# Performance work log

Hardware: AMD Instinct MI355X
Metric: run time of the kernel (lower is better)

Reference implementation:

```python
import jax, jax.numpy as jnp
import numpy as np

N_HEAD, D_MODEL, D_K, D_V = 16, 1024, 64, 64
BATCH, SEQ = 4, 2048


def setup_inputs() -> dict:
    key = jax.random.key(0)
    ks = jax.random.split(key, 9)
    s = 1.0 / np.sqrt(D_MODEL)
    so = 1.0 / np.sqrt(N_HEAD * D_V)
    inp = {
        "input": jax.random.normal(ks[0], (BATCH, SEQ, D_MODEL), jnp.float32),
        # causal mask: True => masked (set to -inf), matching masked_fill semantics
        "attn_mask": jnp.triu(jnp.ones((SEQ, SEQ), bool), k=1),
        "Wq": jax.random.uniform(ks[1], (D_MODEL, N_HEAD * D_K), jnp.float32, -s, s),
        "bq": jax.random.uniform(ks[2], (N_HEAD * D_K,), jnp.float32, -s, s),
        "Wk": jax.random.uniform(ks[3], (D_MODEL, N_HEAD * D_K), jnp.float32, -s, s),
        "bk": jax.random.uniform(ks[4], (N_HEAD * D_K,), jnp.float32, -s, s),
        "Wv": jax.random.uniform(ks[5], (D_MODEL, N_HEAD * D_V), jnp.float32, -s, s),
        "bv": jax.random.uniform(ks[6], (N_HEAD * D_V,), jnp.float32, -s, s),
        "Wo": jax.random.uniform(ks[7], (N_HEAD * D_V, D_MODEL), jnp.float32, -so, so),
        "bo": jax.random.uniform(ks[8], (D_MODEL,), jnp.float32, -so, so),
    }
    return inp


def reference(input, attn_mask, Wq, bq, Wk, bk, Wv, bv, Wo, bo):
    B, S, _ = input.shape
    scale = 1.0 / np.sqrt(D_K)
    q = (input @ Wq + bq).reshape(B, S, N_HEAD, D_K)  # bshd
    k = (input @ Wk + bk).reshape(B, S, N_HEAD, D_K)
    v = (input @ Wv + bv).reshape(B, S, N_HEAD, D_V)
    # scores [B, H, S, S]
    score = jnp.einsum("bqhd,bkhd->bhqk", q, k) * scale
    score = jnp.where(attn_mask[None, None], -jnp.inf, score)
    prob = jax.nn.softmax(score, axis=-1)
    attn = jnp.einsum("bhqk,bkhd->bqhd", prob, v).reshape(B, S, N_HEAD * D_V)
    return attn @ Wo + bo
```

## Files before the change

### kernel.cpp

```cpp
#include <hip/hip_runtime.h>
#include <math.h>


typedef __attribute__((ext_vector_type(8))) short short8;
typedef __attribute__((ext_vector_type(4))) short s16x4;
typedef __attribute__((ext_vector_type(4))) float f32x4;
typedef __attribute__((ext_vector_type(4))) unsigned short u16x4;

constexpr int B  = 4;
constexpr int S  = 2048;
constexpr int H  = 16;
constexpr int DM = 1024;
constexpr int M  = B * S;

__device__ __forceinline__ unsigned short f2bf(float f) {
    union { float f; unsigned u; } v; v.f = f;
    unsigned r = v.u + 0x7FFFu + ((v.u >> 16) & 1u);
    return (unsigned short)(r >> 16);
}

__device__ __forceinline__ void gload16(const void* g, void* l) {
    __builtin_amdgcn_global_load_lds(
        (const __attribute__((address_space(1))) void*)g,
        (__attribute__((address_space(3))) void*)l, 16, 0, 0);
}

__device__ __forceinline__ f32x4 mfma_16x16x16(s16x4 a, s16x4 b, f32x4 c) {
#if __has_builtin(__builtin_amdgcn_mfma_f32_16x16x16bf16_1k)
    return __builtin_amdgcn_mfma_f32_16x16x16bf16_1k(a, b, c, 0, 0, 0);
#else
    asm("v_mfma_f32_16x16x16_bf16 %0, %1, %2, %0" : "+v"(c) : "v"(a), "v"(b));
    return c;
#endif
}

__global__ __launch_bounds__(256) void cast_x_kernel(
    const float* __restrict__ in, unsigned short* __restrict__ out)
{
    const size_t i = (size_t)blockIdx.x * 256 + threadIdx.x;
    const float4* p = (const float4*)in;
    float4 a = p[2 * i], b = p[2 * i + 1];
    short8 o;
    o[0] = (short)f2bf(a.x); o[1] = (short)f2bf(a.y);
    o[2] = (short)f2bf(a.z); o[3] = (short)f2bf(a.w);
    o[4] = (short)f2bf(b.x); o[5] = (short)f2bf(b.y);
    o[6] = (short)f2bf(b.z); o[7] = (short)f2bf(b.w);
    *(short8*)(out + 8 * i) = o;
}

__global__ __launch_bounds__(256) void transpose_cast_w(
    const float* __restrict__ W, unsigned short* __restrict__ Wt)
{
    __shared__ float tile[32][33];
    const int t = threadIdx.x;
    const int r0 = blockIdx.y * 32, c0 = blockIdx.x * 32;
    {
        const int r = t >> 3, c4 = (t & 7) * 4;
        float4 a = *(const float4*)&W[(size_t)(r0 + r) * 1024 + c0 + c4];
        tile[r][c4 + 0] = a.x; tile[r][c4 + 1] = a.y;
        tile[r][c4 + 2] = a.z; tile[r][c4 + 3] = a.w;
    }
    __syncthreads();
    {
        const int n = t >> 3, k4 = (t & 7) * 4;
        u16x4 o;
        o[0] = f2bf(tile[k4 + 0][n]); o[1] = f2bf(tile[k4 + 1][n]);
        o[2] = f2bf(tile[k4 + 2][n]); o[3] = f2bf(tile[k4 + 3][n]);
        *(u16x4*)&Wt[(size_t)(c0 + n) * 1024 + r0 + k4] = o;
    }
}

template <int MODE>
__global__ __launch_bounds__(256) void gemm_bf16(
    const unsigned short* __restrict__ X, const unsigned short* __restrict__ Wt,
    const float* __restrict__ bias, void* __restrict__ dst, float scale)
{
    __shared__ __align__(16) unsigned short As[128 * 32];
    __shared__ __align__(16) unsigned short Bs[128 * 32];

    const int t = threadIdx.x;
    const int lane = t & 63, w = t >> 6;
    const int wr = w >> 1, wc = w & 1;
    const int l15 = lane & 15, lhi = lane >> 4;
    const int row0 = blockIdx.y * 128, col0 = blockIdx.x * 128;

    const f32x4 z = {0.f, 0.f, 0.f, 0.f};
    f32x4 acc[4][4];
    #pragma unroll
    for (int i = 0; i < 4; ++i)
        #pragma unroll
        for (int j = 0; j < 4; ++j) acc[i][j] = z;

    const int fchunk = ((lhi ^ ((l15 >> 1) & 3)) << 4);

    for (int k0 = 0; k0 < 1024; k0 += 32) {
        __syncthreads();
        #pragma unroll
        for (int i = 0; i < 2; ++i) {
            int seg = t + i * 256;
            int row = seg >> 2;
            int ch  = (seg & 3) ^ ((row >> 1) & 3);
            gload16(X  + (size_t)(row0 + row) * 1024 + k0 + ch * 8, (char*)As + seg * 16);
            gload16(Wt + (size_t)(col0 + row) * 1024 + k0 + ch * 8, (char*)Bs + seg * 16);
        }
        __syncthreads();

        short8 a[4], b[4];
        #pragma unroll
        for (int mi = 0; mi < 4; ++mi)
            a[mi] = *(const short8*)((const char*)As + (wr * 64 + mi * 16 + l15) * 64 + fchunk);
        #pragma unroll
        for (int ni = 0; ni < 4; ++ni)
            b[ni] = *(const short8*)((const char*)Bs + (wc * 64 + ni * 16 + l15) * 64 + fchunk);
        #pragma unroll
        for (int mi = 0; mi < 4; ++mi)
            #pragma unroll
            for (int ni = 0; ni < 4; ++ni)
                acc[mi][ni] = __builtin_amdgcn_mfma_f32_16x16x32_bf16(
                    a[mi], b[ni], acc[mi][ni], 0, 0, 0);
    }

    #pragma unroll
    for (int mi = 0; mi < 4; ++mi)
        #pragma unroll
        for (int ni = 0; ni < 4; ++ni) {
            const int cc = col0 + wc * 64 + ni * 16 + l15;
            const float bv = bias[cc];
            if constexpr (MODE == 2) {
                const int rr0 = row0 + wr * 64 + mi * 16 + lhi * 4;
                const int b0 = rr0 >> 11, s0_ = rr0 & 2047;
                u16x4 pv;
                pv[0] = f2bf(acc[mi][ni][0] + bv);
                pv[1] = f2bf(acc[mi][ni][1] + bv);
                pv[2] = f2bf(acc[mi][ni][2] + bv);
                pv[3] = f2bf(acc[mi][ni][3] + bv);
                *(u16x4*)&((unsigned short*)dst)[
                    (((size_t)(b0 * 16 + (cc >> 6)) * 64 + (cc & 63)) << 11) + s0_] = pv;
            } else {
                #pragma unroll
                for (int r = 0; r < 4; ++r) {
                    const int rr = row0 + wr * 64 + mi * 16 + lhi * 4 + r;
                    const float val = acc[mi][ni][r] + bv;
                    if constexpr (MODE == 0) {
                        ((unsigned short*)dst)[((((size_t)(rr >> 11) * 16 + (cc >> 6)) * 2048
                                                + (rr & 2047)) << 6) + (cc & 63)]
                            = f2bf(val * scale);
                    } else {
                        ((float*)dst)[(size_t)rr * 1024 + cc] = val;
                    }
                }
            }
        }
}

__global__ __launch_bounds__(256) void attn_mfma(
    const unsigned short* __restrict__ Q, const unsigned short* __restrict__ K,
    const unsigned short* __restrict__ Vt, unsigned short* __restrict__ Out)
{
    __shared__ __align__(16) unsigned short Ks[2][64 * 64];
    __shared__ __align__(16) unsigned short Vs[2][64 * 64];

    const int t = threadIdx.x, lane = t & 63, w = t >> 6;
    const int l15 = lane & 15, lhi = lane >> 4;
    const int id = blockIdx.x;
    const int bx = id >> 6, bh = id & 63;
    const int q0 = bx * 128;
    const size_t base = (size_t)bh * S * 64;

    short8 bq[2][2];
    #pragma unroll
    for (int mi = 0; mi < 2; ++mi)
        #pragma unroll
        for (int ks = 0; ks < 2; ++ks)
            bq[mi][ks] = *(const short8*)(Q + base
                + (size_t)(q0 + w * 32 + mi * 16 + l15) * 64 + ks * 32 + lhi * 8);

    const f32x4 z = {0.f, 0.f, 0.f, 0.f};
    f32x4 o[2][4];
    float mrow[2] = {-INFINITY, -INFINITY}, lrow[2] = {0.f, 0.f};
    #pragma unroll
    for (int mi = 0; mi < 2; ++mi)
        #pragma unroll
        for (int d = 0; d < 4; ++d) o[mi][d] = z;

    auto STAGE = [&](int buf, int kt) {
        const int k0 = kt * 64;
        #pragma unroll
        for (int i = 0; i < 2; ++i) {
            int seg = t + i * 256;
            int row = seg >> 3;
            int ch  = (seg & 7) ^ (row & 7);
            gload16(K + base + (size_t)(k0 + row) * 64 + ch * 8,
                    (char*)Ks[buf] + seg * 16);
            gload16(Vt + ((size_t)bh * 64 + row) * S + k0 + ch * 8,
                    (char*)Vs[buf] + seg * 16);
        }
    };

    const int ntiles = 2 * bx + 2;
    STAGE(0, 0);
    __syncthreads();

    for (int kt = 0; kt < ntiles; ++kt) {
        const int cur = kt & 1;
        const int k0 = kt * 64;
        if (kt + 1 < ntiles) STAGE(cur ^ 1, kt + 1);

        f32x4 sc[2][4];
        #pragma unroll
        for (int mi = 0; mi < 2; ++mi)
            #pragma unroll
            for (int ni = 0; ni < 4; ++ni) sc[mi][ni] = z;
        #pragma unroll
        for (int ks = 0; ks < 2; ++ks)
            #pragma unroll
            for (int ni = 0; ni < 4; ++ni) {
                short8 ak = *(const short8*)((const char*)Ks[cur]
                    + (ni * 16 + l15) * 128 + (((ks * 4 + lhi) ^ (l15 & 7)) << 4));
                #pragma unroll
                for (int mi = 0; mi < 2; ++mi)
                    sc[mi][ni] = __builtin_amdgcn_mfma_f32_16x16x32_bf16(
                        ak, bq[mi][ks], sc[mi][ni], 0, 0, 0);
            }

        if (k0 >= q0) {
            #pragma unroll
            for (int mi = 0; mi < 2; ++mi) {
                const int qg = q0 + w * 32 + mi * 16 + l15;
                #pragma unroll
                for (int ni = 0; ni < 4; ++ni)
                    #pragma unroll
                    for (int r = 0; r < 4; ++r)
                        if (k0 + ni * 16 + lhi * 4 + r > qg)
                            sc[mi][ni][r] = -INFINITY;
            }
        }

        s16x4 pf[2][4];
        #pragma unroll
        for (int mi = 0; mi < 2; ++mi) {
            float tm = -INFINITY;
            #pragma unroll
            for (int ni = 0; ni < 4; ++ni) {
                float a0 = fmaxf(sc[mi][ni][0], sc[mi][ni][1]);
                float a1 = fmaxf(sc[mi][ni][2], sc[mi][ni][3]);
                tm = fmaxf(tm, fmaxf(a0, a1));
            }
            tm = fmaxf(tm, __shfl_xor(tm, 16));
            tm = fmaxf(tm, __shfl_xor(tm, 32));
            const float mnew = fmaxf(mrow[mi], tm);
            const float alpha = exp2f(mrow[mi] - mnew);
            mrow[mi] = mnew;
            float ps = 0.f;
            #pragma unroll
            for (int ni = 0; ni < 4; ++ni) {
                #pragma unroll
                for (int r = 0; r < 4; ++r) {
                    float pp = exp2f(sc[mi][ni][r] - mnew);
                    sc[mi][ni][r] = pp;
                    ps += pp;
                }
                s16x4 pk;
                pk[0] = (short)f2bf(sc[mi][ni][0]);
                pk[1] = (short)f2bf(sc[mi][ni][1]);
                pk[2] = (short)f2bf(sc[mi][ni][2]);
                pk[3] = (short)f2bf(sc[mi][ni][3]);
                pf[mi][ni] = pk;
            }
            ps += __shfl_xor(ps, 16);
            ps += __shfl_xor(ps, 32);
            lrow[mi] = lrow[mi] * alpha + ps;
            #pragma unroll
            for (int d = 0; d < 4; ++d) {
                o[mi][d][0] *= alpha; o[mi][d][1] *= alpha;
                o[mi][d][2] *= alpha; o[mi][d][3] *= alpha;
            }
        }

        #pragma unroll
        for (int ni = 0; ni < 4; ++ni) {
            #pragma unroll
            for (int db = 0; db < 4; ++db) {
                const int row = db * 16 + l15;
                const int slot = ((ni * 2 + (lhi >> 1)) ^ (l15 & 7));
                s16x4 av = *(const s16x4*)((const char*)Vs[cur]
                    + row * 128 + slot * 16 + (lhi & 1) * 8);
                #pragma unroll
                for (int mi = 0; mi < 2; ++mi)
                    o[mi][db] = mfma_16x16x16(av, pf[mi][ni], o[mi][db]);
            }
        }

        __syncthreads();
    }

    const int b_ = bh >> 4, h_ = bh & 15;
    #pragma unroll
    for (int mi = 0; mi < 2; ++mi) {
        const float inv = 1.0f / lrow[mi];
        const int s_ = q0 + w * 32 + mi * 16 + l15;
        #pragma unroll
        for (int db = 0; db < 4; ++db) {
            u16x4 ov;
            ov[0] = f2bf(o[mi][db][0] * inv);
            ov[1] = f2bf(o[mi][db][1] * inv);
            ov[2] = f2bf(o[mi][db][2] * inv);
            ov[3] = f2bf(o[mi][db][3] * inv);
            *(u16x4*)&Out[(size_t)(b_ * S + s_) * 1024 + h_ * 64 + db * 16 + lhi * 4] = ov;
        }
    }
}

extern "C" void kernel_launch(void* const* d_in, const int* in_sizes, int n_in,
                              void* d_out, int out_size, void* d_ws, size_t ws_size,
                              hipStream_t stream)
{
    const float* x  = (const float*)d_in[0];
    const float* Wq = (const float*)d_in[2];
    const float* bq = (const float*)d_in[3];
    const float* Wk = (const float*)d_in[4];
    const float* bk = (const float*)d_in[5];
    const float* Wv = (const float*)d_in[6];
    const float* bv = (const float*)d_in[7];
    const float* Wo = (const float*)d_in[8];
    const float* bo = (const float*)d_in[9];
    float* out = (float*)d_out;

    unsigned short* p = (unsigned short*)d_ws;
    unsigned short* xb  = p; p += (size_t)M * DM;
    unsigned short* wqt = p; p += (size_t)DM * DM;
    unsigned short* wkt = p; p += (size_t)DM * DM;
    unsigned short* wvt = p; p += (size_t)DM * DM;
    unsigned short* wot = p; p += (size_t)DM * DM;
    unsigned short* qb  = p; p += (size_t)M * DM;
    unsigned short* kb  = p; p += (size_t)M * DM;
    unsigned short* vtb = p; p += (size_t)M * DM;
    unsigned short* attnb = p;

    cast_x_kernel<<<M * DM / 8 / 256, 256, 0, stream>>>(x, xb);
    transpose_cast_w<<<dim3(32, 32), 256, 0, stream>>>(Wq, wqt);
    transpose_cast_w<<<dim3(32, 32), 256, 0, stream>>>(Wk, wkt);
    transpose_cast_w<<<dim3(32, 32), 256, 0, stream>>>(Wv, wvt);
    transpose_cast_w<<<dim3(32, 32), 256, 0, stream>>>(Wo, wot);

    const float qscale = 0.125f * 1.44269504088896340736f;
    gemm_bf16<0><<<dim3(8, 64), 256, 0, stream>>>(xb, wqt, bq, qb, qscale);
    gemm_bf16<0><<<dim3(8, 64), 256, 0, stream>>>(xb, wkt, bk, kb, 1.0f);
    gemm_bf16<2><<<dim3(8, 64), 256, 0, stream>>>(xb, wvt, bv, vtb, 1.0f);

    attn_mfma<<<dim3(1024), 256, 0, stream>>>(qb, kb, vtb, attnb);

    gemm_bf16<1><<<dim3(8, 64), 256, 0, stream>>>(attnb, wot, bo, out, 1.0f);
}
```

Measured before the change: 351.0 us.

## Fuse QKV projections, double-buffer GEMM, lazy softmax rescale, packed bf16 conversion

Merges the Q, K and V projection GEMMs into one launch over a 3072-wide output. This relies on the three transposed weight buffers sitting next to each other in the workspace, and picks the bias and destination per column range. The four weight transpose launches become one 3D-grid launch. The GEMM main loop now double-buffers its LDS tiles so the next k-slice loads while the current one computes. In attention, the online-softmax rescale of O and l is skipped unless the running max grows by more than 8 in log2 space. Softmax and output bf16 packing use v_cvt_pk_bf16_f32, and the V^T store is swizzled so LDS reads hit fewer bank conflicts. These changes add LDS use per GEMM block and slightly change numerics through lazy rescaling and hardware rounding.

Measured after the change: 314.5 us. 10.4% less time.

```diff
diff --git a/kernel.cpp b/kernel.cpp
--- a/kernel.cpp
+++ b/kernel.cpp
@@ -6,6 +6,7 @@
 typedef __attribute__((ext_vector_type(4))) short s16x4;
 typedef __attribute__((ext_vector_type(4))) float f32x4;
 typedef __attribute__((ext_vector_type(4))) unsigned short u16x4;
+typedef __attribute__((ext_vector_type(2))) unsigned int u32x2;
 
 constexpr int B  = 4;
 constexpr int S  = 2048;
@@ -17,6 +18,14 @@
     union { float f; unsigned u; } v; v.f = f;
     unsigned r = v.u + 0x7FFFu + ((v.u >> 16) & 1u);
     return (unsigned short)(r >> 16);
+}
+
+__device__ __forceinline__ s16x4 pack_bf16x4(float a, float b, float c, float d) {
+    unsigned r0, r1;
+    asm("v_cvt_pk_bf16_f32 %0, %1, %2" : "=v"(r0) : "v"(a), "v"(b));
+    asm("v_cvt_pk_bf16_f32 %0, %1, %2" : "=v"(r1) : "v"(c), "v"(d));
+    u32x2 t; t[0] = r0; t[1] = r1;
+    return __builtin_bit_cast(s16x4, t);
 }
 
 __device__ __forceinline__ void gload16(const void* g, void* l) {
@@ -49,8 +58,15 @@
 }
 
 __global__ __launch_bounds__(256) void transpose_cast_w(
-    const float* __restrict__ W, unsigned short* __restrict__ Wt)
-{
+    const float* __restrict__ W0, const float* __restrict__ W1,
+    const float* __restrict__ W2, const float* __restrict__ W3,
+    unsigned short* __restrict__ T0, unsigned short* __restrict__ T1,
+    unsigned short* __restrict__ T2, unsigned short* __restrict__ T3)
+{
+    const int z = blockIdx.z;
+    const float* W = (z == 0) ? W0 : (z == 1) ? W1 : (z == 2) ? W2 : W3;
+    unsigned short* Wt = (z == 0) ? T0 : (z == 1) ? T1 : (z == 2) ? T2 : T3;
+
     __shared__ float tile[32][33];
     const int t = threadIdx.x;
     const int r0 = blockIdx.y * 32, c0 = blockIdx.x * 32;
@@ -70,13 +86,16 @@
     }
 }
 
-template <int MODE>
+template <int FUSED>
 __global__ __launch_bounds__(256) void gemm_bf16(
     const unsigned short* __restrict__ X, const unsigned short* __restrict__ Wt,
-    const float* __restrict__ bias, void* __restrict__ dst, float scale)
-{
-    __shared__ __align__(16) unsigned short As[128 * 32];
-    __shared__ __align__(16) unsigned short Bs[128 * 32];
+    const float* __restrict__ bias_q, const float* __restrict__ bias_k,
+    const float* __restrict__ bias_v,
+    void* __restrict__ dq, void* __restrict__ dk, void* __restrict__ dv,
+    float qscale)
+{
+    __shared__ __align__(16) unsigned short As[2][128 * 32];
+    __shared__ __align__(16) unsigned short Bs[2][128 * 32];
 
     const int t = threadIdx.x;
     const int lane = t & 63, w = t >> 6;
@@ -93,25 +112,34 @@
 
     const int fchunk = ((lhi ^ ((l15 >> 1) & 3)) << 4);
 
-    for (int k0 = 0; k0 < 1024; k0 += 32) {
-        __syncthreads();
+    auto STAGE = [&](int buf, int k0) {
         #pragma unroll
         for (int i = 0; i < 2; ++i) {
             int seg = t + i * 256;
             int row = seg >> 2;
             int ch  = (seg & 3) ^ ((row >> 1) & 3);
-            gload16(X  + (size_t)(row0 + row) * 1024 + k0 + ch * 8, (char*)As + seg * 16);
-            gload16(Wt + (size_t)(col0 + row) * 1024 + k0 + ch * 8, (char*)Bs + seg * 16);
-        }
+            gload16(X  + (size_t)(row0 + row) * 1024 + k0 + ch * 8,
+                    (char*)As[buf] + seg * 16);
+            gload16(Wt + (size_t)(col0 + row) * 1024 + k0 + ch * 8,
+                    (char*)Bs[buf] + seg * 16);
+        }
+    };
+
+    STAGE(0, 0);
+    for (int k0 = 0; k0 < 1024; k0 += 32) {
+        const int cur = (k0 >> 5) & 1;
         __syncthreads();
+        if (k0 + 32 < 1024) STAGE(cur ^ 1, k0 + 32);
 
         short8 a[4], b[4];
         #pragma unroll
         for (int mi = 0; mi < 4; ++mi)
-            a[mi] = *(const short8*)((const char*)As + (wr * 64 + mi * 16 + l15) * 64 + fchunk);
+            a[mi] = *(const short8*)((const char*)As[cur]
+                + (wr * 64 + mi * 16 + l15) * 64 + fchunk);
         #pragma unroll
         for (int ni = 0; ni < 4; ++ni)
-            b[ni] = *(const short8*)((const char*)Bs + (wc * 64 + ni * 16 + l15) * 64 + fchunk);
+            b[ni] = *(const short8*)((const char*)Bs[cur]
+                + (wc * 64 + ni * 16 + l15) * 64 + fchunk);
         #pragma unroll
         for (int mi = 0; mi < 4; ++mi)
             #pragma unroll
@@ -125,29 +153,34 @@
         #pragma unroll
         for (int ni = 0; ni < 4; ++ni) {
             const int cc = col0 + wc * 64 + ni * 16 + l15;
-            const float bv = bias[cc];
-            if constexpr (MODE == 2) {
+            if constexpr (FUSED == 1) {
+                const int sel = cc >> 10;
+                const int hh = (cc >> 6) & 15, dd = cc & 63;
+                const float bv = (sel == 0 ? bias_q : sel == 1 ? bias_k : bias_v)
+                                 [cc & 1023];
                 const int rr0 = row0 + wr * 64 + mi * 16 + lhi * 4;
-                const int b0 = rr0 >> 11, s0_ = rr0 & 2047;
-                u16x4 pv;
-                pv[0] = f2bf(acc[mi][ni][0] + bv);
-                pv[1] = f2bf(acc[mi][ni][1] + bv);
-                pv[2] = f2bf(acc[mi][ni][2] + bv);
-                pv[3] = f2bf(acc[mi][ni][3] + bv);
-                *(u16x4*)&((unsigned short*)dst)[
-                    (((size_t)(b0 * 16 + (cc >> 6)) * 64 + (cc & 63)) << 11) + s0_] = pv;
+                const int b0i = rr0 >> 11, s0_ = rr0 & 2047;
+                if (sel == 2) {
+                    const int sstore = s0_ ^ (((cc >> 3) & 1) << 2);
+                    s16x4 pv = pack_bf16x4(
+                        acc[mi][ni][0] + bv, acc[mi][ni][1] + bv,
+                        acc[mi][ni][2] + bv, acc[mi][ni][3] + bv);
+                    *(s16x4*)&((unsigned short*)dv)[
+                        (((size_t)(b0i * 16 + hh) * 64 + dd) << 11) + sstore] = pv;
+                } else {
+                    unsigned short* dst = (unsigned short*)(sel == 0 ? dq : dk);
+                    const float sc_ = (sel == 0) ? qscale : 1.0f;
+                    #pragma unroll
+                    for (int r = 0; r < 4; ++r)
+                        dst[(((size_t)(b0i * 16 + hh) * 2048 + s0_ + r) << 6) + dd]
+                            = f2bf((acc[mi][ni][r] + bv) * sc_);
+                }
             } else {
+                const float bv = bias_q[cc];
                 #pragma unroll
                 for (int r = 0; r < 4; ++r) {
                     const int rr = row0 + wr * 64 + mi * 16 + lhi * 4 + r;
-                    const float val = acc[mi][ni][r] + bv;
-                    if constexpr (MODE == 0) {
-                        ((unsigned short*)dst)[((((size_t)(rr >> 11) * 16 + (cc >> 6)) * 2048
-                                                + (rr & 2047)) << 6) + (cc & 63)]
-                            = f2bf(val * scale);
-                    } else {
-                        ((float*)dst)[(size_t)rr * 1024 + cc] = val;
-                    }
+                    ((float*)dq)[(size_t)rr * 1024 + cc] = acc[mi][ni][r] + bv;
                 }
             }
         }
@@ -248,33 +281,30 @@
             }
             tm = fmaxf(tm, __shfl_xor(tm, 16));
             tm = fmaxf(tm, __shfl_xor(tm, 32));
-            const float mnew = fmaxf(mrow[mi], tm);
-            const float alpha = exp2f(mrow[mi] - mnew);
-            mrow[mi] = mnew;
+            if (!__all(tm <= mrow[mi] + 8.f)) {
+                const float mnew = fmaxf(mrow[mi], tm);
+                const float alpha = exp2f(mrow[mi] - mnew);
+                mrow[mi] = mnew;
+                lrow[mi] *= alpha;
+                #pragma unroll
+                for (int d = 0; d < 4; ++d) {
+                    o[mi][d][0] *= alpha; o[mi][d][1] *= alpha;
+                    o[mi][d][2] *= alpha; o[mi][d][3] *= alpha;
+                }
+            }
             float ps = 0.f;
             #pragma unroll
             for (int ni = 0; ni < 4; ++ni) {
-                #pragma unroll
-                for (int r = 0; r < 4; ++r) {
-                    float pp = exp2f(sc[mi][ni][r] - mnew);
-                    sc[mi][ni][r] = pp;
-                    ps += pp;
-                }
-                s16x4 pk;
-                pk[0] = (short)f2bf(sc[mi][ni][0]);
-                pk[1] = (short)f2bf(sc[mi][ni][1]);
-                pk[2] = (short)f2bf(sc[mi][ni][2]);
-                pk[3] = (short)f2bf(sc[mi][ni][3]);
-                pf[mi][ni] = pk;
+                float p0 = exp2f(sc[mi][ni][0] - mrow[mi]);
+                float p1 = exp2f(sc[mi][ni][1] - mrow[mi]);
+                float p2 = exp2f(sc[mi][ni][2] - mrow[mi]);
+                float p3 = exp2f(sc[mi][ni][3] - mrow[mi]);
+                ps += (p0 + p1) + (p2 + p3);
+                pf[mi][ni] = pack_bf16x4(p0, p1, p2, p3);
             }
             ps += __shfl_xor(ps, 16);
             ps += __shfl_xor(ps, 32);
-            lrow[mi] = lrow[mi] * alpha + ps;
-            #pragma unroll
-            for (int d = 0; d < 4; ++d) {
-                o[mi][d][0] *= alpha; o[mi][d][1] *= alpha;
-                o[mi][d][2] *= alpha; o[mi][d][3] *= alpha;
-            }
+            lrow[mi] += ps;
         }
 
         #pragma unroll
@@ -283,8 +313,9 @@
             for (int db = 0; db < 4; ++db) {
                 const int row = db * 16 + l15;
                 const int slot = ((ni * 2 + (lhi >> 1)) ^ (l15 & 7));
+                const int half = (lhi & 1) ^ ((l15 >> 3) & 1);
                 s16x4 av = *(const s16x4*)((const char*)Vs[cur]
-                    + row * 128 + slot * 16 + (lhi & 1) * 8);
+                    + row * 128 + slot * 16 + half * 8);
                 #pragma unroll
                 for (int mi = 0; mi < 2; ++mi)
                     o[mi][db] = mfma_16x16x16(av, pf[mi][ni], o[mi][db]);
@@ -301,12 +332,10 @@
         const int s_ = q0 + w * 32 + mi * 16 + l15;
         #pragma unroll
         for (int db = 0; db < 4; ++db) {
-            u16x4 ov;
-            ov[0] = f2bf(o[mi][db][0] * inv);
-            ov[1] = f2bf(o[mi][db][1] * inv);
-            ov[2] = f2bf(o[mi][db][2] * inv);
-            ov[3] = f2bf(o[mi][db][3] * inv);
-            *(u16x4*)&Out[(size_t)(b_ * S + s_) * 1024 + h_ * 64 + db * 16 + lhi * 4] = ov;
+            s16x4 ov = pack_bf16x4(o[mi][db][0] * inv, o[mi][db][1] * inv,
+                                   o[mi][db][2] * inv, o[mi][db][3] * inv);
+            *(s16x4*)&Out[(size_t)(b_ * S + s_) * 1024 + h_ * 64 + db * 16 + lhi * 4]
+                = ov;
         }
     }
 }
@@ -338,17 +367,15 @@
     unsigned short* attnb = p;
 
     cast_x_kernel<<<M * DM / 8 / 256, 256, 0, stream>>>(x, xb);
-    transpose_cast_w<<<dim3(32, 32), 256, 0, stream>>>(Wq, wqt);
-    transpose_cast_w<<<dim3(32, 32), 256, 0, stream>>>(Wk, wkt);
-    transpose_cast_w<<<dim3(32, 32), 256, 0, stream>>>(Wv, wvt);
-    transpose_cast_w<<<dim3(32, 32), 256, 0, stream>>>(Wo, wot);
+    transpose_cast_w<<<dim3(32, 32, 4), 256, 0, stream>>>(
+        Wq, Wk, Wv, Wo, wqt, wkt, wvt, wot);
 
     const float qscale = 0.125f * 1.44269504088896340736f;
-    gemm_bf16<0><<<dim3(8, 64), 256, 0, stream>>>(xb, wqt, bq, qb, qscale);
-    gemm_bf16<0><<<dim3(8, 64), 256, 0, stream>>>(xb, wkt, bk, kb, 1.0f);
-    gemm_bf16<2><<<dim3(8, 64), 256, 0, stream>>>(xb, wvt, bv, vtb, 1.0f);
+    gemm_bf16<1><<<dim3(24, 64), 256, 0, stream>>>(
+        xb, wqt, bq, bk, bv, qb, kb, vtb, qscale);
 
     attn_mfma<<<dim3(1024), 256, 0, stream>>>(qb, kb, vtb, attnb);
 
-    gemm_bf16<1><<<dim3(8, 64), 256, 0, stream>>>(attnb, wot, bo, out, 1.0f);
-}
+    gemm_bf16<0><<<dim3(8, 64), 256, 0, stream>>>(
+        attnb, wot, bo, nullptr, nullptr, out, nullptr, nullptr, 1.0f);
+}
```
